# Kernel tuning notes

Hardware: AMD Instinct MI355X
Metric: run time of the kernel (lower is better)

## Reference

```python
import jax, jax.numpy as jnp
import numpy as np

L, HID, NH, DH, OUT = 20, 512, 8, 64, 1000
NPAT, PS = 14, 16
IN_DIM = 3 * PS * PS          # 768
SEQ = NPAT * NPAT + 1         # 197
BATCH = 64
EPS = 1e-5


def _pos_embeddings(seq_len, d):
    # sin(i/10000^(j/d)) for even j, cos(i/10000^((j-1)/d)) for odd j
    i = jnp.arange(seq_len, dtype=jnp.float32)[:, None]
    j = jnp.arange(d)
    je = (j - (j % 2)).astype(jnp.float32)
    ang = i / jnp.power(10000.0, je / d)
    return jnp.where(j % 2 == 0, jnp.sin(ang), jnp.cos(ang))


def _layernorm(x, g, b):
    m = jnp.mean(x, axis=-1, keepdims=True)
    v = jnp.mean(jnp.square(x - m), axis=-1, keepdims=True)
    return (x - m) * jax.lax.rsqrt(v + EPS) * g + b


def setup_inputs() -> dict:
    key = jax.random.key(0)
    ks = jax.random.split(key, 12)
    r = lambda k, sh: jax.random.normal(k, sh, dtype=jnp.float32) * 0.02
    return {
        "x": jax.random.normal(ks[0], (BATCH, 3, 224, 224), dtype=jnp.float32),
        "embed_W": r(ks[1], (IN_DIM, HID)),
        "embed_b": jnp.zeros((HID,), jnp.float32),
        "cls": r(ks[2], (HID,)),
        "ln1_g": jnp.ones((L, HID), jnp.float32),
        "ln1_b": jnp.zeros((L, HID), jnp.float32),
        "qW": r(ks[3], (L, NH, DH, DH)),
        "qb": jnp.zeros((L, NH, DH), jnp.float32),
        "kW": r(ks[4], (L, NH, DH, DH)),
        "kb": jnp.zeros((L, NH, DH), jnp.float32),
        "vW": r(ks[5], (L, NH, DH, DH)),
        "vb": jnp.zeros((L, NH, DH), jnp.float32),
        "ln2_g": jnp.ones((L, HID), jnp.float32),
        "ln2_b": jnp.zeros((L, HID), jnp.float32),
        "mlp1_W": r(ks[6], (L, HID, 4 * HID)),
        "mlp1_b": jnp.zeros((L, 4 * HID), jnp.float32),
        "mlp2_W": r(ks[7], (L, 4 * HID, HID)),
        "mlp2_b": jnp.zeros((L, HID), jnp.float32),
        "head_W": r(ks[8], (HID, OUT)),
        "head_b": jnp.zeros((OUT,), jnp.float32),
    }


def reference(x, embed_W, embed_b, cls, ln1_g, ln1_b, qW, qb, kW, kb, vW, vb,
              ln2_g, ln2_b, mlp1_W, mlp1_b, mlp2_W, mlp2_b, head_W, head_b):
    n = x.shape[0]
    # patchify: [n,3,224,224] -> [n,196,768], flatten order (c, ph, pw)
    p = x.reshape(n, 3, NPAT, PS, NPAT, PS)
    p = p.transpose(0, 2, 4, 1, 3, 5).reshape(n, NPAT * NPAT, IN_DIM)
    tokens = p @ embed_W + embed_b                      # [n,196,HID]
    cls_tok = jnp.broadcast_to(cls, (n, 1, HID))
    h = jnp.concatenate([cls_tok, tokens], axis=1)      # [n,197,HID]
    h = h + _pos_embeddings(SEQ, HID)

    scale = 1.0 / jnp.sqrt(jnp.float32(DH))

    def step(h, params):
        (g1, b1, qw, qb_, kw, kb_, vw, vb_, g2, b2, w1, b1m, w2, b2m) = params
        y = _layernorm(h, g1, b1)                       # [n,S,HID]
        yh = y.reshape(n, SEQ, NH, DH)
        # torch Linear: out = seq @ W.T + b; qw stored as [NH, out, in]
        q = jnp.einsum('nshd,hed->nshe', yh, qw) + qb_
        k = jnp.einsum('nshd,hed->nshe', yh, kw) + kb_
        v = jnp.einsum('nshd,hed->nshe', yh, vw) + vb_
        att = jax.nn.softmax(jnp.einsum('nqhd,nkhd->nhqk', q, k) * scale, axis=-1)
        o = jnp.einsum('nhqk,nkhd->nqhd', att, v).reshape(n, SEQ, HID)
        h = h + o
        z = _layernorm(h, g2, b2)
        z = jax.nn.gelu(z @ w1 + b1m, approximate=False) @ w2 + b2m
        return h + z, None

    params = (ln1_g, ln1_b, qW, qb, kW, kb, vW, vb,
              ln2_g, ln2_b, mlp1_W, mlp1_b, mlp2_W, mlp2_b)
    h, _ = jax.lax.scan(step, h, params)
    logits = h[:, 0] @ head_W + head_b
    return jax.nn.softmax(logits, axis=-1)
```

## Files before the change

### kernel.cpp

```cpp
#include <hip/hip_runtime.h>
#include <hip/hip_bf16.h>
#include <math.h>

#define LAY 20
#define HID 512
#define NH 8
#define DH 64
#define OUTC 1000
#define SEQ 197
#define SPAD 224
#define BATCH 64
#define TT (BATCH*SEQ)
#define M2 12800
#define NPTOK (BATCH*196)
#define IN_DIM 768

typedef __attribute__((ext_vector_type(8))) short bf16x8;
typedef __attribute__((ext_vector_type(4))) float f32x4;

__device__ __forceinline__ ushort f2bf(float f){
  __hip_bfloat16 h = __float2bfloat16(f);
  return *(ushort*)&h;
}
__device__ __forceinline__ float bf2f(ushort u){
  __hip_bfloat16 h = *(__hip_bfloat16*)&u;
  return __bfloat162float(h);
}

__device__ __forceinline__ float posemb(int i, int j){
  float je = (float)(j & ~1);
  float ang = (float)i * powf(10000.0f, -je * (1.0f/(float)HID));
  return (j & 1) ? cosf(ang) : sinf(ang);
}

__device__ __forceinline__ float gelu_exact(float x){
  return 0.5f * x * (1.0f + erff(x * 0.70710678118654752f));
}

__device__ __forceinline__ void gld_lds16(const ushort* g, ushort* l){
  __builtin_amdgcn_global_load_lds((const __attribute__((address_space(1))) void*)g,
                                   (__attribute__((address_space(3))) void*)l, 16, 0, 0);
}

__global__ __launch_bounds__(512)
void pos_kernel(float* __restrict__ pos){
  int i = blockIdx.x, j = threadIdx.x;
  pos[(size_t)i*HID + j] = posemb(i, j);
}

__global__ __launch_bounds__(256)
void convt_kernel(const float* __restrict__ src, ushort* __restrict__ dst,
                  int R, int C){
  __shared__ float tile[32][33];
  const float* s = src + (size_t)blockIdx.z * R * C;
  ushort* d      = dst + (size_t)blockIdx.z * R * C;
  int r0 = blockIdx.y * 32, c0 = blockIdx.x * 32;
  int tc = threadIdx.x & 31, tr = threadIdx.x >> 5;
  #pragma unroll
  for (int i = 0; i < 4; ++i)
    tile[tr + i*8][tc] = s[(size_t)(r0 + tr + i*8)*C + c0 + tc];
  __syncthreads();
  #pragma unroll
  for (int i = 0; i < 4; ++i)
    d[(size_t)(c0 + tr + i*8)*R + r0 + tc] = f2bf(tile[tc][tr + i*8]);
}

__global__ __launch_bounds__(256)
void cvt_kernel(const float* __restrict__ src, ushort* __restrict__ dst, int count){
  int idx = blockIdx.x * 256 + threadIdx.x;
  if (idx < count) dst[idx] = f2bf(src[idx]);
}

__global__ __launch_bounds__(256)
void patchify_kernel(const float* __restrict__ x, ushort* __restrict__ p){
  int idx = blockIdx.x * 256 + threadIdx.x;
  int r   = idx / 768, cdx = idx - r * 768;
  int n   = r / 196,  pp  = r - n * 196;
  int pr  = pp / 14,  pc  = pp - pr * 14;
  int c   = cdx >> 8, rem = cdx & 255;
  int ph  = rem >> 4, pw  = rem & 15;
  p[idx] = f2bf(x[ (((size_t)(n*3 + c)*224) + pr*16 + ph)*224 + pc*16 + pw ]);
}

__global__ __launch_bounds__(512)
void cls_kernel(const float* __restrict__ cls, const float* __restrict__ pos,
                float* __restrict__ h){
  int n = blockIdx.x, e = threadIdx.x;
  h[(size_t)n*SEQ*HID + e] = cls[e] + pos[e];
}

template<int BM, int WM, int WN, int EPI>
__global__ __launch_bounds__(WM*WN*64, 2)
void gemm_pipe(const ushort* __restrict__ A, const ushort* __restrict__ Bt,
               const float* __restrict__ bias, void* __restrict__ Cv,
               int K, int N, int Mreal, int NBX, const float* __restrict__ pos){
  constexpr int BN = BM;
  constexpr int THREADS = WM*WN*64;
  static_assert(THREADS == BM*2, "stage mapping requires THREADS==2*BM");
  constexpr int PWM = BM/WM, PWN = BN/WN;
  constexpr int MF = PWM/16, NF = PWN/16, MFQ = MF/4;
  static_assert(MFQ*4 == MF, "");
  static_assert(PWN == 64 && NF == 4, "epilogue assumes 64-col wave region");
  __shared__ char lds[2*2*BM*128];

  int t = threadIdx.x, lane = t & 63, wave = t >> 6;
  int wr = wave / WN, wn = wave % WN;
  int l16 = lane & 15, g = lane >> 4;

  int NB = gridDim.x;
  int q8 = NB >> 3, r8 = NB & 7;
  int xcd = blockIdx.x & 7, i8 = blockIdx.x >> 3;
  int swz = (xcd < r8 ? xcd*(q8+1) : r8*(q8+1) + (xcd-r8)*q8) + i8;
  int rb = (swz / NBX) * BM, cb = (swz % NBX) * BN;

  const int srow8 = t >> 3, sslot = t & 7;

  f32x4 acc[MF][NF];
  #pragma unroll
  for (int mf = 0; mf < MF; ++mf)
    #pragma unroll
    for (int nf = 0; nf < NF; ++nf)
      acc[mf][nf] = (f32x4){0.f,0.f,0.f,0.f};

#define STAGE(qq, kt, db) do{                                                  \
    int row_ = (qq)*(BM/4) + srow8;                                            \
    int kel_ = (sslot ^ (row_ & 7)) * 8;                                       \
    char* b_ = lds + (db)*(2*BM*128);                                          \
    gld_lds16(A  + (size_t)(rb+row_)*K + (kt)*64 + kel_,                       \
              (ushort*)(b_ + (qq)*(BM*32) + t*16));                            \
    gld_lds16(Bt + (size_t)(cb+row_)*K + (kt)*64 + kel_,                       \
              (ushort*)(b_ + BM*128 + (qq)*(BM*32) + t*16));                   \
  }while(0)

#define RDF(db, isB, row, kc)                                                  \
  (*(const bf16x8*)(lds + (db)*(2*BM*128) + (isB)*(BM*128) + (row)*128 +       \
                    ((((kc)*4 + g) ^ ((row) & 7)) << 4)))

  #pragma unroll
  for (int q = 0; q < 4; ++q) STAGE(q, 0, 0);

  int NT = K / 64;
  for (int tt = 0; tt < NT; ++tt){
    int db = tt & 1, dn = db ^ 1;
    bool pf = (tt + 1 < NT);
    if (pf){
      #pragma unroll
      for (int q = 0; q < 4; ++q) STAGE(q, tt+1, dn);
      asm volatile("s_waitcnt vmcnt(8)" ::: "memory");
    } else {
      asm volatile("s_waitcnt vmcnt(0)" ::: "memory");
    }
    __builtin_amdgcn_s_barrier();

    bf16x8 bf[NF][2];
    #pragma unroll
    for (int nf = 0; nf < NF; ++nf)
      #pragma unroll
      for (int kc = 0; kc < 2; ++kc)
        bf[nf][kc] = RDF(db, 1, wn*PWN + nf*16 + l16, kc);

    #pragma unroll
    for (int q = 0; q < 4; ++q){
      bf16x8 af[MFQ][2];
      #pragma unroll
      for (int mq = 0; mq < MFQ; ++mq)
        #pragma unroll
        for (int kc = 0; kc < 2; ++kc)
          af[mq][kc] = RDF(db, 0, wr*PWM + (q*MFQ + mq)*16 + l16, kc);
      __builtin_amdgcn_s_setprio(1);
      #pragma unroll
      for (int mq = 0; mq < MFQ; ++mq)
        #pragma unroll
        for (int nf = 0; nf < NF; ++nf)
          #pragma unroll
          for (int kc = 0; kc < 2; ++kc)
            acc[q*MFQ + mq][nf] = __builtin_amdgcn_mfma_f32_16x16x32_bf16(af[mq][kc], bf[nf][kc], acc[q*MFQ + mq][nf], 0, 0, 0);
      __builtin_amdgcn_s_setprio(0);
    }
    __builtin_amdgcn_s_barrier();
  }
#undef STAGE
#undef RDF

  float bvv[NF];
  #pragma unroll
  for (int nf = 0; nf < NF; ++nf)
    bvv[nf] = bias[cb + wn*PWN + nf*16 + l16];
  float* eps = (float*)(lds + wave*(16*76*4));

  #pragma unroll
  for (int mf = 0; mf < MF; ++mf){
    #pragma unroll
    for (int nf = 0; nf < NF; ++nf)
      #pragma unroll
      for (int j = 0; j < 4; ++j){
        float val = acc[mf][nf][j] + bvv[nf];
        if (EPI == 1) val = gelu_exact(val);
        eps[(g*4+j)*76 + nf*16 + l16] = val;
      }
    #pragma unroll
    for (int i = 0; i < 4; ++i){
      int id = i*64 + lane;
      int r = id >> 4, c4 = id & 15;
      float4 vv = *(float4*)&eps[r*76 + c4*4];
      int grow = rb + wr*PWM + mf*16 + r;
      int gcol = cb + wn*PWN + c4*4;
      if (EPI == 1){
        ushort4 u;
        u.x = f2bf(vv.x); u.y = f2bf(vv.y); u.z = f2bf(vv.z); u.w = f2bf(vv.w);
        *(ushort4*)&((ushort*)Cv)[(size_t)grow*N + gcol] = u;
      } else if (EPI == 2){
        if (grow < Mreal){
          float* cp = &((float*)Cv)[(size_t)grow*N + gcol];
          float4 o = *(float4*)cp;
          o.x += vv.x; o.y += vv.y; o.z += vv.z; o.w += vv.w;
          *(float4*)cp = o;
        }
      } else {
        if (grow < Mreal){
          int bn = grow / 196, sp = grow - bn*196;
          float4 pv = *(const float4*)&pos[(size_t)(1+sp)*HID + gcol];
          vv.x += pv.x; vv.y += pv.y; vv.z += pv.z; vv.w += pv.w;
          *(float4*)&((float*)Cv)[((size_t)bn*SEQ + 1 + sp)*HID + gcol] = vv;
        }
      }
    }
  }
}

__global__ __launch_bounds__(256)
void ln_kernel(const float* __restrict__ x, const float* __restrict__ g,
               const float* __restrict__ b, ushort* __restrict__ y){
  int tok = blockIdx.x, t = threadIdx.x;
  const float* xp = x + (size_t)tok*HID;
  float v1 = xp[t], v2 = xp[t + 256];
  __shared__ float red[4];
  float s = v1 + v2;
  #pragma unroll
  for (int off = 32; off; off >>= 1) s += __shfl_xor(s, off);
  if ((t & 63) == 0) red[t >> 6] = s;
  __syncthreads();
  float mean = (red[0] + red[1] + red[2] + red[3]) * (1.0f/512.0f);
  __syncthreads();
  float d1 = v1 - mean, d2 = v2 - mean;
  s = d1*d1 + d2*d2;
  #pragma unroll
  for (int off = 32; off; off >>= 1) s += __shfl_xor(s, off);
  if ((t & 63) == 0) red[t >> 6] = s;
  __syncthreads();
  float var = (red[0] + red[1] + red[2] + red[3]) * (1.0f/512.0f);
  float rs  = rsqrtf(var + 1e-5f);
  ushort* yp = y + (size_t)tok*HID;
  yp[t]       = f2bf(d1*rs*g[t]       + b[t]);
  yp[t + 256] = f2bf(d2*rs*g[t + 256] + b[t + 256]);
}

__global__ __launch_bounds__(256)
void qkv_mfma(const ushort* __restrict__ y,
              const ushort* __restrict__ wqb, const ushort* __restrict__ wkb,
              const ushort* __restrict__ wvb,
              const float* __restrict__ bq, const float* __restrict__ bk,
              const float* __restrict__ bv,
              ushort* __restrict__ q, ushort* __restrict__ k,
              ushort* __restrict__ v){
  __shared__ short As[128*64];
  __shared__ short Bs[64*64];
  int t = threadIdx.x;
  int lane = t & 63, wave = t >> 6;
  int l16 = lane & 15, g = lane >> 4;
  int p  = blockIdx.y >> 3, hh = blockIdx.y & 7;
  int rb = blockIdx.x * 128;

  const ushort* W; const float* bias; ushort* out;
  if (p == 0)      { W = wqb; bias = bq; out = q; }
  else if (p == 1) { W = wkb; bias = bk; out = k; }
  else             { W = wvb; bias = bv; out = v; }
  W    += (size_t)hh * 64 * 64;
  bias += hh * 64;

  int srow = t >> 3, skoff = (t & 7) * 8;
  const ushort* Ab = y + (size_t)(rb + srow)*HID + hh*64 + skoff;
  const ushort* Bb = W + (size_t)srow*64 + skoff;
  #pragma unroll
  for (int i = 0; i < 4; ++i)
    gld_lds16(Ab + (size_t)(i*32)*HID, (ushort*)&As[t*8 + i*2048]);
  #pragma unroll
  for (int i = 0; i < 2; ++i)
    gld_lds16(Bb + (size_t)(i*32)*64, (ushort*)&Bs[t*8 + i*2048]);
  __syncthreads();

  f32x4 acc[2][4];
  #pragma unroll
  for (int m = 0; m < 2; ++m)
    #pragma unroll
    for (int n = 0; n < 4; ++n)
      acc[m][n] = (f32x4){0.f,0.f,0.f,0.f};

  #pragma unroll
  for (int kc = 0; kc < 2; ++kc){
    bf16x8 af[2], bfr[4];
    #pragma unroll
    for (int m = 0; m < 2; ++m)
      af[m] = *(bf16x8*)&As[(wave*32 + m*16 + l16)*64 + kc*32 + g*8];
    #pragma unroll
    for (int n = 0; n < 4; ++n)
      bfr[n] = *(bf16x8*)&Bs[(n*16 + l16)*64 + kc*32 + g*8];
    #pragma unroll
    for (int m = 0; m < 2; ++m)
      #pragma unroll
      for (int n = 0; n < 4; ++n)
        acc[m][n] = __builtin_amdgcn_mfma_f32_16x16x32_bf16(af[m], bfr[n], acc[m][n], 0, 0, 0);
  }
  __syncthreads();

  float bvv[4];
  #pragma unroll
  for (int nd = 0; nd < 4; ++nd) bvv[nd] = bias[nd*16 + l16];
  ushort* eps = (ushort*)As + wave*(16*72);
  #pragma unroll
  for (int mch = 0; mch < 2; ++mch){
    #pragma unroll
    for (int nd = 0; nd < 4; ++nd)
      #pragma unroll
      for (int j = 0; j < 4; ++j)
        eps[(g*4+j)*72 + nd*16 + l16] = f2bf(acc[mch][nd][j] + bvv[nd]);
    #pragma unroll
    for (int i = 0; i < 2; ++i){
      int id = i*64 + lane;
      int r = id >> 3, c8 = id & 7;
      uint4 vv = *(uint4*)&eps[r*72 + c8*8];
      int tok = rb + wave*32 + mch*16 + r;
      if (tok < TT)
        *(uint4*)&out[(size_t)tok*HID + hh*64 + c8*8] = vv;
    }
  }
}

__global__ __launch_bounds__(512, 4)
void attn_kernel(const ushort* __restrict__ q, const ushort* __restrict__ k,
                 const ushort* __restrict__ v, float* __restrict__ h){
  __shared__ ushort Ks[SPAD*64];
  __shared__ ushort Vs[64*256];
  __shared__ ushort Ps[8][32*40];
  int nh = blockIdx.x;
  int n = nh >> 3, hd = nh & 7;
  int t = threadIdx.x;
  int lane = t & 63, wave = t >> 6;
  int l16 = lane & 15, g = lane >> 4;

  const ushort* kbase = k + ((size_t)n*SEQ)*HID + hd*64;
  for (int c = t; c < 224*8; c += 512){
    int s = c >> 3, c8 = (c & 7) * 8;
    int sr = s < SEQ ? s : SEQ-1;
    uint4 val = *(const uint4*)&kbase[(size_t)sr*HID + c8];
    int byte = s*128 + c8*2;
    byte ^= (s & 7) << 4;
    *(uint4*)((char*)Ks + byte) = val;
  }
  const ushort* vbase = v + ((size_t)n*SEQ)*HID + hd*64;
  for (int c = t; c < 224*8; c += 512){
    int s = c >> 3, d8 = (c & 7) * 8;
    uint4 val = {0u,0u,0u,0u};
    if (s < SEQ) val = *(const uint4*)&vbase[(size_t)s*HID + d8];
    ushort* vsp = (ushort*)Vs;
    #pragma unroll
    for (int e = 0; e < 8; ++e){
      int d = d8 + e;
      int swzi = ((d & 7) ^ ((d >> 3) & 7)) << 4;
      int byte = d*512 + ((s*2) ^ swzi);
      vsp[byte >> 1] = ((ushort*)&val)[e];
    }
  }

  int qrow0 = wave * 32;
  bool wactive = qrow0 < SEQ;
  bf16x8 aq[2][2];
  if (wactive){
    #pragma unroll
    for (int m = 0; m < 2; ++m){
      int row = qrow0 + m*16 + l16;
      int sr = row < SEQ ? row : SEQ-1;
      const ushort* qp = q + ((size_t)n*SEQ + sr)*HID + hd*64;
      #pragma unroll
      for (int kc = 0; kc < 2; ++kc)
        aq[m][kc] = *(const bf16x8*)&qp[kc*32 + g*8];
    }
  }
  __syncthreads();

  if (wactive){
    ushort* myP = &Ps[wave][0];
    f32x4 accO[2][4];
    float mrun[2][4], lrun[2][4];
    #pragma unroll
    for (int m = 0; m < 2; ++m){
      #pragma unroll
      for (int nd = 0; nd < 4; ++nd) accO[m][nd] = (f32x4){0.f,0.f,0.f,0.f};
      #pragma unroll
      for (int j = 0; j < 4; ++j){ mrun[m][j] = -1e30f; lrun[m][j] = 0.f; }
    }

    for (int kt = 0; kt < 7; ++kt){
      f32x4 accS[2][2];
      #pragma unroll
      for (int m = 0; m < 2; ++m)
        #pragma unroll
        for (int nn = 0; nn < 2; ++nn) accS[m][nn] = (f32x4){0.f,0.f,0.f,0.f};
      #pragma unroll
      for (int kc = 0; kc < 2; ++kc){
        bf16x8 bk[2];
        #pragma unroll
        for (int nn = 0; nn < 2; ++nn){
          int srow = kt*32 + nn*16 + l16;
          int byte = srow*128 + kc*64 + g*16;
          byte ^= (srow & 7) << 4;
          bk[nn] = *(const bf16x8*)((const char*)Ks + byte);
        }
        #pragma unroll
        for (int m = 0; m < 2; ++m)
          #pragma unroll
          for (int nn = 0; nn < 2; ++nn)
            accS[m][nn] = __builtin_amdgcn_mfma_f32_16x16x32_bf16(aq[m][kc], bk[nn], accS[m][nn], 0, 0, 0);
      }
      bool kv0 = (kt*32 + l16) < SEQ;
      bool kv1 = (kt*32 + 16 + l16) < SEQ;
      #pragma unroll
      for (int m = 0; m < 2; ++m){
        #pragma unroll
        for (int j = 0; j < 4; ++j){
          float s0 = kv0 ? accS[m][0][j]*0.125f : -1e30f;
          float s1 = kv1 ? accS[m][1][j]*0.125f : -1e30f;
          float mx = fmaxf(s0, s1);
          mx = fmaxf(mx, __shfl_xor(mx, 1));
          mx = fmaxf(mx, __shfl_xor(mx, 2));
          mx = fmaxf(mx, __shfl_xor(mx, 4));
          mx = fmaxf(mx, __shfl_xor(mx, 8));
          float mold = mrun[m][j];
          float mnew = fmaxf(mold, mx);
          float corr = __expf(mold - mnew);
          mrun[m][j] = mnew;
          float p0 = __expf(s0 - mnew);
          float p1 = __expf(s1 - mnew);
          float rs = p0 + p1;
          rs += __shfl_xor(rs, 1);
          rs += __shfl_xor(rs, 2);
          rs += __shfl_xor(rs, 4);
          rs += __shfl_xor(rs, 8);
          lrun[m][j] = lrun[m][j]*corr + rs;
          #pragma unroll
          for (int nd = 0; nd < 4; ++nd) accO[m][nd][j] *= corr;
          int prow = m*16 + g*4 + j;
          myP[prow*40 + l16]      = f2bf(p0);
          myP[prow*40 + 16 + l16] = f2bf(p1);
        }
      }
      bf16x8 ap[2], bv[4];
      #pragma unroll
      for (int m = 0; m < 2; ++m)
        ap[m] = *(const bf16x8*)&myP[(m*16 + l16)*40 + g*8];
      #pragma unroll
      for (int nd = 0; nd < 4; ++nd){
        int d = nd*16 + l16;
        int byte = d*512 + kt*64 + g*16;
        byte ^= ((d & 7) ^ ((d >> 3) & 7)) << 4;
        bv[nd] = *(const bf16x8*)((const char*)Vs + byte);
      }
      #pragma unroll
      for (int m = 0; m < 2; ++m)
        #pragma unroll
        for (int nd = 0; nd < 4; ++nd)
          accO[m][nd] = __builtin_amdgcn_mfma_f32_16x16x32_bf16(ap[m], bv[nd], accO[m][nd], 0, 0, 0);
    }

    #pragma unroll
    for (int m = 0; m < 2; ++m){
      #pragma unroll
      for (int j = 0; j < 4; ++j){
        int row = qrow0 + m*16 + g*4 + j;
        if (row < SEQ){
          float inv = 1.0f / lrun[m][j];
          float* hp = h + ((size_t)n*SEQ + row)*HID + hd*64;
          #pragma unroll
          for (int nd = 0; nd < 4; ++nd)
            hp[nd*16 + l16] += accO[m][nd][j] * inv;
        }
      }
    }
  }
}

__global__ __launch_bounds__(256)
void head_logits(const float* __restrict__ h, const float* __restrict__ W,
                 const float* __restrict__ b, float* __restrict__ logits){
  int c0 = blockIdx.x * 8;
  __shared__ float Ws[512*8];
  int t = threadIdx.x;
  for (int i = t; i < 512*8; i += 256){
    int kx = i >> 3, c = i & 7;
    Ws[i] = W[(size_t)kx*OUTC + c0 + c];
  }
  __syncthreads();
  int n = t >> 2, g = t & 3;
  const float* hp = h + (size_t)n*SEQ*HID + g*128;
  float acc[8] = {};
  for (int kx = 0; kx < 128; ++kx){
    float hv = hp[kx];
    const float* wsr = &Ws[(g*128 + kx)*8];
    #pragma unroll
    for (int c = 0; c < 8; ++c) acc[c] += hv * wsr[c];
  }
  #pragma unroll
  for (int c = 0; c < 8; ++c){
    acc[c] += __shfl_xor(acc[c], 1);
    acc[c] += __shfl_xor(acc[c], 2);
  }
  if (g == 0){
    #pragma unroll
    for (int c = 0; c < 8; ++c)
      logits[(size_t)n*OUTC + c0 + c] = acc[c] + b[c0 + c];
  }
}

__global__ __launch_bounds__(256)
void head_softmax(const float* __restrict__ logits, float* __restrict__ out){
  int n = blockIdx.x, t = threadIdx.x;
  __shared__ float red[4];
  float v[4];
  #pragma unroll
  for (int j = 0; j < 4; ++j){
    int e = t + j*256;
    v[j] = (e < OUTC) ? logits[(size_t)n*OUTC + e] : -1e30f;
  }
  float mx = fmaxf(fmaxf(v[0], v[1]), fmaxf(v[2], v[3]));
  #pragma unroll
  for (int off = 32; off; off >>= 1) mx = fmaxf(mx, __shfl_xor(mx, off));
  if ((t & 63) == 0) red[t >> 6] = mx;
  __syncthreads();
  mx = fmaxf(fmaxf(red[0], red[1]), fmaxf(red[2], red[3]));
  __syncthreads();
  float sum = 0.f;
  #pragma unroll
  for (int j = 0; j < 4; ++j){ v[j] = __expf(v[j] - mx); sum += v[j]; }
  #pragma unroll
  for (int off = 32; off; off >>= 1) sum += __shfl_xor(sum, off);
  if ((t & 63) == 0) red[t >> 6] = sum;
  __syncthreads();
  sum = red[0] + red[1] + red[2] + red[3];
  float inv = 1.0f / sum;
  #pragma unroll
  for (int j = 0; j < 4; ++j){
    int e = t + j*256;
    if (e < OUTC) out[(size_t)n*OUTC + e] = v[j] * inv;
  }
}

extern "C" void kernel_launch(void* const* d_in, const int* in_sizes, int n_in,
                              void* d_out, int out_size, void* d_ws, size_t ws_size,
                              hipStream_t stream){
  const float* x       = (const float*)d_in[0];
  const float* embed_W = (const float*)d_in[1];
  const float* embed_b = (const float*)d_in[2];
  const float* cls     = (const float*)d_in[3];
  const float* ln1_g   = (const float*)d_in[4];
  const float* ln1_b   = (const float*)d_in[5];
  const float* qW      = (const float*)d_in[6];
  const float* qb      = (const float*)d_in[7];
  const float* kW      = (const float*)d_in[8];
  const float* kb      = (const float*)d_in[9];
  const float* vW      = (const float*)d_in[10];
  const float* vb      = (const float*)d_in[11];
  const float* ln2_g   = (const float*)d_in[12];
  const float* ln2_b   = (const float*)d_in[13];
  const float* mlp1_W  = (const float*)d_in[14];
  const float* mlp1_b  = (const float*)d_in[15];
  const float* mlp2_W  = (const float*)d_in[16];
  const float* mlp2_b  = (const float*)d_in[17];
  const float* head_W  = (const float*)d_in[18];
  const float* head_b  = (const float*)d_in[19];
  float* out = (float*)d_out;

  char* wsb = (char*)d_ws;
  float*  h   = (float*)wsb;
  ushort* y   = (ushort*)(wsb + (size_t)M2*HID*4);
  float*  logits = (float*)y;
  char*   un  = wsb + (size_t)M2*HID*4 + (size_t)M2*HID*2;
  ushort* qb_  = (ushort*)un;
  ushort* kb_  = qb_ + (size_t)TT*HID;
  ushort* vb_  = kb_ + (size_t)TT*HID;
  ushort* z1  = (ushort*)un;
  ushort* p   = (ushort*)un;
  char*   wts = un + (size_t)3*TT*HID*4;
  ushort* w1t = (ushort*)wts;
  ushort* w2t = w1t + (size_t)LAY*2048*512;
  ushort* wet = w2t + (size_t)LAY*2048*512;
  ushort* wqb = wet + (size_t)IN_DIM*HID;
  ushort* wkb = wqb + (size_t)LAY*NH*DH*DH;
  ushort* wvb = wkb + (size_t)LAY*NH*DH*DH;
  float*  pos = (float*)(wvb + (size_t)LAY*NH*DH*DH);

  pos_kernel<<<SEQ, 512, 0, stream>>>(pos);
  convt_kernel<<<dim3(2048/32, 512/32, LAY), 256, 0, stream>>>(mlp1_W, w1t, 512, 2048);
  convt_kernel<<<dim3(512/32, 2048/32, LAY), 256, 0, stream>>>(mlp2_W, w2t, 2048, 512);
  convt_kernel<<<dim3(512/32, 768/32, 1),    256, 0, stream>>>(embed_W, wet, 768, 512);
  {
    int cnt = LAY*NH*DH*DH;
    int grd = (cnt + 255)/256;
    cvt_kernel<<<grd, 256, 0, stream>>>(qW, wqb, cnt);
    cvt_kernel<<<grd, 256, 0, stream>>>(kW, wkb, cnt);
    cvt_kernel<<<grd, 256, 0, stream>>>(vW, wvb, cnt);
  }

  patchify_kernel<<<(NPTOK*IN_DIM)/256, 256, 0, stream>>>(x, p);
  cls_kernel<<<BATCH, 512, 0, stream>>>(cls, pos, h);
  gemm_pipe<128, 2, 2, 3><<<(512/128)*(M2/128), 256, 0, stream>>>(
      p, wet, embed_b, h, IN_DIM, HID, NPTOK, 512/128, pos);

  for (int l = 0; l < LAY; ++l){
    ln_kernel<<<TT, 256, 0, stream>>>(h, ln1_g + l*HID, ln1_b + l*HID, y);
    qkv_mfma<<<dim3(M2/128, 24), 256, 0, stream>>>(
        y,
        wqb + (size_t)l*NH*DH*DH, wkb + (size_t)l*NH*DH*DH, wvb + (size_t)l*NH*DH*DH,
        qb + (size_t)l*HID, kb + (size_t)l*HID, vb + (size_t)l*HID,
        qb_, kb_, vb_);
    attn_kernel<<<BATCH*NH, 512, 0, stream>>>(qb_, kb_, vb_, h);
    ln_kernel<<<TT, 256, 0, stream>>>(h, ln2_g + l*HID, ln2_b + l*HID, y);
    gemm_pipe<256, 2, 4, 1><<<(2048/256)*(M2/256), 512, 0, stream>>>(
        y, w1t + (size_t)l*2048*512, mlp1_b + (size_t)l*4*HID, z1,
        HID, 4*HID, TT, 2048/256, pos);
    gemm_pipe<128, 2, 2, 2><<<(512/128)*(M2/128), 256, 0, stream>>>(
        z1, w2t + (size_t)l*2048*512, mlp2_b + (size_t)l*HID, h,
        4*HID, HID, TT, 512/128, pos);
  }

  head_logits<<<125, 256, 0, stream>>>(h, head_W, head_b, logits);
  head_softmax<<<BATCH, 256, 0, stream>>>(logits, out);
}
```

Measured before the change: 3.431 ms.

## Rework GEMM to fixed 128x128 tiles with 32-wide K steps and smaller LDS

The templated GEMM becomes a single 128x128 tile, 4-wave kernel. It stages K in chunks of 32 instead of 64, drops the XOR swizzle, and precomputes the global and LDS offsets. LDS use shrinks to 32 KB and launch bounds rise to 4 blocks per CU to raise occupancy, and the MLP1 GEMM switches from 256x256 tiles to this config. In exchange there are twice as many barriers per K, less reuse per tile for MLP1, and likely LDS bank conflicts because the swizzle is gone.

```diff
diff --git a/kernel.cpp b/kernel.cpp
--- a/kernel.cpp
+++ b/kernel.cpp
@@ -89,22 +89,18 @@
   h[(size_t)n*SEQ*HID + e] = cls[e] + pos[e];
 }
 
-template<int BM, int WM, int WN, int EPI>
-__global__ __launch_bounds__(WM*WN*64, 2)
+template<int EPI>
+__global__ __launch_bounds__(256, 4)
 void gemm_pipe(const ushort* __restrict__ A, const ushort* __restrict__ Bt,
                const float* __restrict__ bias, void* __restrict__ Cv,
                int K, int N, int Mreal, int NBX, const float* __restrict__ pos){
-  constexpr int BN = BM;
-  constexpr int THREADS = WM*WN*64;
-  static_assert(THREADS == BM*2, "stage mapping requires THREADS==2*BM");
-  constexpr int PWM = BM/WM, PWN = BN/WN;
-  constexpr int MF = PWM/16, NF = PWN/16, MFQ = MF/4;
-  static_assert(MFQ*4 == MF, "");
-  static_assert(PWN == 64 && NF == 4, "epilogue assumes 64-col wave region");
-  __shared__ char lds[2*2*BM*128];
+  constexpr int BM = 128, BN = 128;
+  constexpr int MF = 4, NF = 4;
+  constexpr int TBS = 16384;
+  __shared__ char lds[2*TBS];
 
   int t = threadIdx.x, lane = t & 63, wave = t >> 6;
-  int wr = wave / WN, wn = wave % WN;
+  int wr = wave >> 1, wn = wave & 1;
   int l16 = lane & 15, g = lane >> 4;
 
   int NB = gridDim.x;
@@ -113,7 +109,22 @@
   int swz = (xcd < r8 ? xcd*(q8+1) : r8*(q8+1) + (xcd-r8)*q8) + i8;
   int rb = (swz / NBX) * BM, cb = (swz % NBX) * BN;
 
-  const int srow8 = t >> 3, sslot = t & 7;
+  const int srow = t >> 2, sslot = t & 3;
+  const ushort* pA[2]; const ushort* pB[2];
+  #pragma unroll
+  for (int q = 0; q < 2; ++q){
+    pA[q] = A  + (size_t)(rb + q*64 + srow)*K + sslot*8;
+    pB[q] = Bt + (size_t)(cb + q*64 + srow)*K + sslot*8;
+  }
+  const int sdst = t*16;
+
+  int aoff[MF], boff[NF];
+  #pragma unroll
+  for (int mf = 0; mf < MF; ++mf)
+    aoff[mf] = (wr*64 + mf*16 + l16)*64 + g*16;
+  #pragma unroll
+  for (int nf = 0; nf < NF; ++nf)
+    boff[nf] = 8192 + (wn*64 + nf*16 + l16)*64 + g*16;
 
   f32x4 acc[MF][NF];
   #pragma unroll
@@ -122,70 +133,52 @@
     for (int nf = 0; nf < NF; ++nf)
       acc[mf][nf] = (f32x4){0.f,0.f,0.f,0.f};
 
-#define STAGE(qq, kt, db) do{                                                  \
-    int row_ = (qq)*(BM/4) + srow8;                                            \
-    int kel_ = (sslot ^ (row_ & 7)) * 8;                                       \
-    char* b_ = lds + (db)*(2*BM*128);                                          \
-    gld_lds16(A  + (size_t)(rb+row_)*K + (kt)*64 + kel_,                       \
-              (ushort*)(b_ + (qq)*(BM*32) + t*16));                            \
-    gld_lds16(Bt + (size_t)(cb+row_)*K + (kt)*64 + kel_,                       \
-              (ushort*)(b_ + BM*128 + (qq)*(BM*32) + t*16));                   \
-  }while(0)
-
-#define RDF(db, isB, row, kc)                                                  \
-  (*(const bf16x8*)(lds + (db)*(2*BM*128) + (isB)*(BM*128) + (row)*128 +       \
-                    ((((kc)*4 + g) ^ ((row) & 7)) << 4)))
-
-  #pragma unroll
-  for (int q = 0; q < 4; ++q) STAGE(q, 0, 0);
-
-  int NT = K / 64;
+  #pragma unroll
+  for (int q = 0; q < 2; ++q){
+    gld_lds16(pA[q], (ushort*)(lds + q*4096 + sdst));
+    gld_lds16(pB[q], (ushort*)(lds + 8192 + q*4096 + sdst));
+  }
+
+  int NT = K / 32;
   for (int tt = 0; tt < NT; ++tt){
-    int db = tt & 1, dn = db ^ 1;
+    const char* cur = lds + (tt & 1)*TBS;
+    char* nxt = lds + ((tt & 1) ^ 1)*TBS;
     bool pf = (tt + 1 < NT);
     if (pf){
-      #pragma unroll
-      for (int q = 0; q < 4; ++q) STAGE(q, tt+1, dn);
-      asm volatile("s_waitcnt vmcnt(8)" ::: "memory");
+      const size_t kb = (size_t)(tt + 1) * 32;
+      #pragma unroll
+      for (int q = 0; q < 2; ++q){
+        gld_lds16(pA[q] + kb, (ushort*)(nxt + q*4096 + sdst));
+        gld_lds16(pB[q] + kb, (ushort*)(nxt + 8192 + q*4096 + sdst));
+      }
+      asm volatile("s_waitcnt vmcnt(4)" ::: "memory");
     } else {
       asm volatile("s_waitcnt vmcnt(0)" ::: "memory");
     }
     __builtin_amdgcn_s_barrier();
 
-    bf16x8 bf[NF][2];
+    bf16x8 af[MF], bfr[NF];
     #pragma unroll
     for (int nf = 0; nf < NF; ++nf)
-      #pragma unroll
-      for (int kc = 0; kc < 2; ++kc)
-        bf[nf][kc] = RDF(db, 1, wn*PWN + nf*16 + l16, kc);
-
-    #pragma unroll
-    for (int q = 0; q < 4; ++q){
-      bf16x8 af[MFQ][2];
-      #pragma unroll
-      for (int mq = 0; mq < MFQ; ++mq)
-        #pragma unroll
-        for (int kc = 0; kc < 2; ++kc)
-          af[mq][kc] = RDF(db, 0, wr*PWM + (q*MFQ + mq)*16 + l16, kc);
-      __builtin_amdgcn_s_setprio(1);
-      #pragma unroll
-      for (int mq = 0; mq < MFQ; ++mq)
-        #pragma unroll
-        for (int nf = 0; nf < NF; ++nf)
-          #pragma unroll
-          for (int kc = 0; kc < 2; ++kc)
-            acc[q*MFQ + mq][nf] = __builtin_amdgcn_mfma_f32_16x16x32_bf16(af[mq][kc], bf[nf][kc], acc[q*MFQ + mq][nf], 0, 0, 0);
-      __builtin_amdgcn_s_setprio(0);
-    }
+      bfr[nf] = *(const bf16x8*)(cur + boff[nf]);
+    #pragma unroll
+    for (int mf = 0; mf < MF; ++mf)
+      af[mf] = *(const bf16x8*)(cur + aoff[mf]);
+
+    __builtin_amdgcn_s_setprio(1);
+    #pragma unroll
+    for (int mf = 0; mf < MF; ++mf)
+      #pragma unroll
+      for (int nf = 0; nf < NF; ++nf)
+        acc[mf][nf] = __builtin_amdgcn_mfma_f32_16x16x32_bf16(af[mf], bfr[nf], acc[mf][nf], 0, 0, 0);
+    __builtin_amdgcn_s_setprio(0);
     __builtin_amdgcn_s_barrier();
   }
-#undef STAGE
-#undef RDF
 
   float bvv[NF];
   #pragma unroll
   for (int nf = 0; nf < NF; ++nf)
-    bvv[nf] = bias[cb + wn*PWN + nf*16 + l16];
+    bvv[nf] = bias[cb + wn*64 + nf*16 + l16];
   float* eps = (float*)(lds + wave*(16*76*4));
 
   #pragma unroll
@@ -203,8 +196,8 @@
       int id = i*64 + lane;
       int r = id >> 4, c4 = id & 15;
       float4 vv = *(float4*)&eps[r*76 + c4*4];
-      int grow = rb + wr*PWM + mf*16 + r;
-      int gcol = cb + wn*PWN + c4*4;
+      int grow = rb + wr*64 + mf*16 + r;
+      int gcol = cb + wn*64 + c4*4;
       if (EPI == 1){
         ushort4 u;
         u.x = f2bf(vv.x); u.y = f2bf(vv.y); u.z = f2bf(vv.z); u.w = f2bf(vv.w);
@@ -612,7 +605,7 @@
 
   patchify_kernel<<<(NPTOK*IN_DIM)/256, 256, 0, stream>>>(x, p);
   cls_kernel<<<BATCH, 512, 0, stream>>>(cls, pos, h);
-  gemm_pipe<128, 2, 2, 3><<<(512/128)*(M2/128), 256, 0, stream>>>(
+  gemm_pipe<3><<<(512/128)*(M2/128), 256, 0, stream>>>(
       p, wet, embed_b, h, IN_DIM, HID, NPTOK, 512/128, pos);
 
   for (int l = 0; l < LAY; ++l){
@@ -624,10 +617,10 @@
         qb_, kb_, vb_);
     attn_kernel<<<BATCH*NH, 512, 0, stream>>>(qb_, kb_, vb_, h);
     ln_kernel<<<TT, 256, 0, stream>>>(h, ln2_g + l*HID, ln2_b + l*HID, y);
-    gemm_pipe<256, 2, 4, 1><<<(2048/256)*(M2/256), 512, 0, stream>>>(
+    gemm_pipe<1><<<(2048/128)*(M2/128), 256, 0, stream>>>(
         y, w1t + (size_t)l*2048*512, mlp1_b + (size_t)l*4*HID, z1,
-        HID, 4*HID, TT, 2048/256, pos);
-    gemm_pipe<128, 2, 2, 2><<<(512/128)*(M2/128), 256, 0, stream>>>(
+        HID, 4*HID, TT, 2048/128, pos);
+    gemm_pipe<2><<<(512/128)*(M2/128), 256, 0, stream>>>(
         z1, w2t + (size_t)l*2048*512, mlp2_b + (size_t)l*HID, h,
         4*HID, HID, TT, 512/128, pos);
   }
```

Measured after the change: 3.327 ms. 1.03x faster.
